# Kernel optimization log

Measured on AMD Instinct MI355X. Metric: run time of the kernel, lower is better.

The kernel has to match this reference:

```python
import jax, jax.numpy as jnp
import numpy as np

B, N, D, H = 8, 512, 512, 8
DK = D // H          # 64
DIM_G = 64           # trigonometric geometry embedding dim
WAVE_LEN = 1000.0


def box_relational_embedding(f_g):
    # f_g: [B, N, 4] -> [B, N, N, 64]
    x_min, y_min, x_max, y_max = [f_g[..., i] for i in range(4)]  # [B,N]
    cx = (x_min + x_max) * 0.5
    cy = (y_min + y_max) * 0.5
    w = x_max - x_min + 1.0
    h = y_max - y_min + 1.0
    # pairwise deltas; divide by w_i / h_i of the row box (broadcast over j)
    dx = jnp.log(jnp.clip(jnp.abs((cx[:, :, None] - cx[:, None, :]) / w[:, :, None]), 0.001))
    dy = jnp.log(jnp.clip(jnp.abs((cy[:, :, None] - cy[:, None, :]) / h[:, :, None]), 0.001))
    dw = jnp.log(w[:, :, None] / w[:, None, :])
    dh = jnp.log(h[:, :, None] / h[:, None, :])
    pos = jnp.stack([dx, dy, dw, dh], axis=-1)  # [B,N,N,4]
    feat_range = jnp.arange(DIM_G // 8, dtype=jnp.float32) / (DIM_G / 8.0)  # [8]
    dim_mat = 1.0 / (WAVE_LEN ** feat_range)  # [8]
    mul = (100.0 * pos)[..., None] * dim_mat  # [B,N,N,4,8]
    mul = mul.reshape(pos.shape[0], pos.shape[1], pos.shape[2], -1)  # [B,N,N,32]
    return jnp.concatenate([jnp.sin(mul), jnp.cos(mul)], axis=-1)  # [B,N,N,64]


def setup_inputs() -> dict:
    key = jax.random.key(0)
    ks = jax.random.split(key, 12)
    s = 1.0 / np.sqrt(D)
    return {
        "input_query": jax.random.normal(ks[0], (B, N, D), jnp.float32),
        "input_key": jax.random.normal(ks[1], (B, N, D), jnp.float32),
        "input_value": jax.random.normal(ks[2], (B, N, D), jnp.float32),
        "input_box": jax.random.uniform(ks[3], (B, N, 4), jnp.float32),
        "mask": jax.random.randint(ks[4], (B, N), 0, 2, jnp.int32),
        "not_objects": jax.random.randint(ks[5], (B, N), 0, 2).astype(jnp.bool_),
        "Wq": jax.random.normal(ks[6], (D, D), jnp.float32) * s,
        "bq": jnp.zeros((D,), jnp.float32),
        "Wk": jax.random.normal(ks[7], (D, D), jnp.float32) * s,
        "bk": jnp.zeros((D,), jnp.float32),
        "Wv": jax.random.normal(ks[8], (D, D), jnp.float32) * s,
        "bv": jnp.zeros((D,), jnp.float32),
        "Wo": jax.random.normal(ks[9], (D, D), jnp.float32) * s,
        "bo": jnp.zeros((D,), jnp.float32),
        "WG": jax.random.normal(ks[10], (H, DIM_G), jnp.float32) * 0.1,
        "bG": jnp.zeros((H,), jnp.float32),
    }


def reference(input_query, input_key, input_value, input_box, mask, not_objects,
              Wq, bq, Wk, bk, Wv, bv, Wo, bo, WG, bG):
    emb = box_relational_embedding(input_box)  # [B,N,N,64]

    def proj(x, W, b):
        return (x @ W + b).reshape(B, N, H, DK).transpose(0, 2, 1, 3)  # [B,H,N,DK]

    q = proj(input_query, Wq, bq)
    k = proj(input_key, Wk, bk)
    v = proj(input_value, Wv, bv)

    scores = jnp.einsum('bhnd,bhmd->bhnm', q, k) / np.sqrt(DK).astype(np.float32)
    scores = jnp.where(mask[:, None, None, :] == 0, -1e9, scores)

    # per-head geometry weights: [B,H,N,N]
    wg = jax.nn.relu(jnp.einsum('bnmg,hg->bhnm', emb, WG) + bG[None, :, None, None])

    # object mask: zero the geometry log-bias where either i or j is not an object
    pair_not_obj = not_objects[:, None, :, None] | not_objects[:, None, None, :]  # [B,1,N,N]
    mask_obj = 1.0 - pair_not_obj.astype(jnp.float32)

    logits = jnp.log(jnp.clip(wg, 1e-6)) * mask_obj + scores
    attn = jax.nn.softmax(logits, axis=-1)  # dropout is identity in eval mode

    out = jnp.einsum('bhnm,bhmd->bhnd', attn, v)
    out = out.transpose(0, 2, 1, 3).reshape(B, N, D)
    return out @ Wo + bo
```

## Files before the change

### kernel.cpp

```cpp
#include <hip/hip_runtime.h>
#include <hip/hip_fp16.h>

#define B_ 8
#define N_ 512
#define D_ 512
#define H_ 8
#define DK_ 64

typedef unsigned int uint;
typedef unsigned short ushort;
typedef __attribute__((ext_vector_type(8))) short short8;
typedef __attribute__((ext_vector_type(8))) _Float16 half8;
typedef __attribute__((ext_vector_type(4))) _Float16 half4;
typedef __attribute__((ext_vector_type(4))) float floatx4;

__device__ __forceinline__ float bf2f(ushort s) { return __uint_as_float(((uint)s) << 16); }
__device__ __forceinline__ ushort f2bf(float f) {
    uint x = __float_as_uint(f);
    return (ushort)((x + 0x7fffu + ((x >> 16) & 1u)) >> 16);
}
__device__ __forceinline__ float blo(uint u) { return __uint_as_float(u << 16); }
__device__ __forceinline__ float bhi(uint u) { return __uint_as_float(u & 0xffff0000u); }
__device__ __forceinline__ float ldf(const void* p, size_t i, int isbf) {
    return isbf ? bf2f(((const ushort*)p)[i]) : ((const float*)p)[i];
}
__device__ __forceinline__ short ldb(const void* p, size_t i, int isbf) {
    return isbf ? (short)(((const ushort*)p)[i]) : (short)f2bf(((const float*)p)[i]);
}
__device__ __forceinline__ float4 ldbox(const void* p, size_t row, int isbf) {
    if (isbf) {
        const uint2 u = ((const uint2*)p)[row];
        return make_float4(blo(u.x), bhi(u.x), blo(u.y), bhi(u.y));
    }
    return ((const float4*)p)[row];
}
__device__ __forceinline__ float flog(float x) {
    return __builtin_amdgcn_logf(x) * 0.69314718056f;
}
__device__ __forceinline__ float fexp(float x) {
    return __builtin_amdgcn_exp2f(x * 1.44269504089f);
}
__device__ __forceinline__ void fsincos_rev(float rev, float* s, float* c) {
    const float fr = rev - floorf(rev);
    *s = __builtin_amdgcn_sinf(fr);
    *c = __builtin_amdgcn_cosf(fr);
}
__device__ __forceinline__ uint pkbf(uint a, uint b) {
    return __builtin_amdgcn_perm(b + 0x8000u, a + 0x8000u, 0x07060302u);
}

__global__ __launch_bounds__(256) void probe_dtype(const uint* __restrict__ q,
                                                   int* __restrict__ flag) {
    __shared__ int s[256];
    const int t = threadIdx.x;
    int cnt = 0;
    for (int i = t; i < 4096; i += 256) {
        const uint e = (q[i] >> 7) & 0xffu;
        cnt += (e >= 0x70u && e <= 0x84u) ? 1 : 0;
    }
    s[t] = cnt;
    __syncthreads();
    for (int d = 128; d > 0; d >>= 1) {
        if (t < d) s[t] += s[t + d];
        __syncthreads();
    }
    if (t == 0) *flag = (s[0] > 3276) ? 1 : 0;
}

__global__ __launch_bounds__(256) void transw(const void* __restrict__ w0,
                                              const void* __restrict__ w1,
                                              const void* __restrict__ w2,
                                              const void* __restrict__ w3,
                                              const void* __restrict__ b0,
                                              const void* __restrict__ b1,
                                              const void* __restrict__ b2,
                                              const void* __restrict__ b3,
                                              ushort* __restrict__ wt,
                                              float* __restrict__ biasf,
                                              const int* __restrict__ flagp) {
    const int isbf = *flagp;
    const int z = blockIdx.z;
    const void* W = (z == 0) ? w0 : (z == 1) ? w1 : (z == 2) ? w2 : w3;
    const int n0 = blockIdx.x * 32, k0 = blockIdx.y * 32;
    __shared__ float tile[32][33];
    const int tx = threadIdx.x & 31, ty = threadIdx.x >> 5;
#pragma unroll
    for (int r = 0; r < 4; ++r)
        tile[ty + 8 * r][tx] = ldf(W, (size_t)(k0 + ty + 8 * r) * D_ + n0 + tx, isbf);
    if (blockIdx.x == 0 && blockIdx.y == 0) {
        const void* bz = (z == 0) ? b0 : (z == 1) ? b1 : (z == 2) ? b2 : b3;
        for (int e = threadIdx.x; e < 512; e += 256)
            biasf[z * 512 + e] = ldf(bz, e, isbf);
    }
    __syncthreads();
#pragma unroll
    for (int r = 0; r < 4; ++r)
        wt[(size_t)z * 262144 + (size_t)(n0 + ty + 8 * r) * D_ + k0 + tx] =
            f2bf(tile[tx][ty + 8 * r]);
}

__global__ __launch_bounds__(256) void stage1(
    const void* __restrict__ xq, const void* __restrict__ xk, const void* __restrict__ xv,
    const ushort* __restrict__ wt, const float* __restrict__ biasf,
    ushort* __restrict__ oq, ushort* __restrict__ ok, ushort* __restrict__ ov,
    const void* __restrict__ box, const int* __restrict__ nobj,
    const void* __restrict__ WG, const void* __restrict__ bG,
    ushort* __restrict__ glog, const int* __restrict__ flagp) {
    __shared__ __align__(16) char smem[22336];
    const int isbf = *flagp;
    const int bid = blockIdx.x;
    const int t = threadIdx.x, wv = t >> 6, lane = t & 63;
    const int m16 = lane & 15, quad = lane >> 4;

    if (bid < 768) {
        const int z = bid >> 8, rem = bid & 255;
        const int row0 = (rem & 31) * 128, col0 = (rem >> 5) * 64;
        const char* A = (const char*)((z == 0) ? xq : (z == 1) ? xk : xv);
        const ushort* W = wt + (size_t)z * 262144;
        const float* bias = biasf + z * 512;
        ushort (*As)[40] = (ushort(*)[40])smem;
        ushort (*Ws)[40] = (ushort(*)[40])(smem + 10240);
        floatx4 acc[2][4] = {};

        const int ar = t >> 1, ah = t & 1;
        const int wr = t >> 2, wc = (t & 3) * 8;

        uint4 ua, ub, uc, ud;
        short8 ps0, ps1, pw;

        auto loadA = [&](int k0) {
            const size_t e = (size_t)(row0 + ar) * D_ + k0 + ah * 16;
            if (isbf) {
                ps0 = *(const short8*)(A + 2 * e);
                ps1 = *(const short8*)(A + 2 * e + 16);
            } else {
                const uint* ap = (const uint*)A + e;
                ua = *(const uint4*)(ap);
                ub = *(const uint4*)(ap + 4);
                uc = *(const uint4*)(ap + 8);
                ud = *(const uint4*)(ap + 12);
            }
            pw = *(const short8*)(W + (size_t)(col0 + wr) * D_ + k0 + wc);
        };
        auto stage = [&]() {
            if (isbf) {
                *(short8*)&As[ar][ah * 16] = ps0;
                *(short8*)&As[ar][ah * 16 + 8] = ps1;
            } else {
                uint4 lo, hi;
                lo.x = pkbf(ua.x, ua.y); lo.y = pkbf(ua.z, ua.w);
                lo.z = pkbf(ub.x, ub.y); lo.w = pkbf(ub.z, ub.w);
                hi.x = pkbf(uc.x, uc.y); hi.y = pkbf(uc.z, uc.w);
                hi.z = pkbf(ud.x, ud.y); hi.w = pkbf(ud.z, ud.w);
                *(uint4*)&As[ar][ah * 16] = lo;
                *(uint4*)&As[ar][ah * 16 + 8] = hi;
            }
            *(short8*)&Ws[wr][wc] = pw;
        };

        loadA(0);
        for (int k0 = 0; k0 < D_; k0 += 32) {
            __syncthreads();
            stage();
            __syncthreads();
            if (k0 + 32 < D_) loadA(k0 + 32);

            const short8 a0 = *(const short8*)&As[wv * 32 + m16][quad * 8];
            const short8 a1 = *(const short8*)&As[wv * 32 + 16 + m16][quad * 8];
            const short8 b0 = *(const short8*)&Ws[m16][quad * 8];
            const short8 b1 = *(const short8*)&Ws[16 + m16][quad * 8];
            const short8 b2 = *(const short8*)&Ws[32 + m16][quad * 8];
            const short8 b3 = *(const short8*)&Ws[48 + m16][quad * 8];
            acc[0][0] = __builtin_amdgcn_mfma_f32_16x16x32_bf16(a0, b0, acc[0][0], 0, 0, 0);
            acc[0][1] = __builtin_amdgcn_mfma_f32_16x16x32_bf16(a0, b1, acc[0][1], 0, 0, 0);
            acc[0][2] = __builtin_amdgcn_mfma_f32_16x16x32_bf16(a0, b2, acc[0][2], 0, 0, 0);
            acc[0][3] = __builtin_amdgcn_mfma_f32_16x16x32_bf16(a0, b3, acc[0][3], 0, 0, 0);
            acc[1][0] = __builtin_amdgcn_mfma_f32_16x16x32_bf16(a1, b0, acc[1][0], 0, 0, 0);
            acc[1][1] = __builtin_amdgcn_mfma_f32_16x16x32_bf16(a1, b1, acc[1][1], 0, 0, 0);
            acc[1][2] = __builtin_amdgcn_mfma_f32_16x16x32_bf16(a1, b2, acc[1][2], 0, 0, 0);
            acc[1][3] = __builtin_amdgcn_mfma_f32_16x16x32_bf16(a1, b3, acc[1][3], 0, 0, 0);
        }

#pragma unroll
        for (int mt = 0; mt < 2; ++mt) {
#pragma unroll
            for (int nt = 0; nt < 4; ++nt) {
                const int colg = col0 + nt * 16 + m16;
                const float bi = bias[colg];
                const float v0 = acc[mt][nt][0] + bi, v1 = acc[mt][nt][1] + bi;
                const float v2 = acc[mt][nt][2] + bi, v3 = acc[mt][nt][3] + bi;
                const int rowb = row0 + wv * 32 + mt * 16 + quad * 4;
                if (z == 2) {
                    const int bhv = (rowb >> 9) * H_ + (colg >> 6);
                    uint2 pk;
                    pk.x = (uint)f2bf(v0) | ((uint)f2bf(v1) << 16);
                    pk.y = (uint)f2bf(v2) | ((uint)f2bf(v3) << 16);
                    *(uint2*)(ov + ((size_t)bhv * DK_ + (colg & 63)) * N_ + (rowb & 511)) = pk;
                } else {
                    ushort* o = (z == 0) ? oq : ok;
                    const float vv[4] = {v0, v1, v2, v3};
#pragma unroll
                    for (int r = 0; r < 4; ++r) {
                        const int row = rowb + r;
                        o[((size_t)((row >> 9) * H_ + (colg >> 6)) * N_ + (row & 511)) * DK_ +
                          (colg & 63)] = f2bf(vv[r]);
                    }
                }
            }
        }
    } else {
        const int id = bid - 768;
        const int i = id & 511, bl = id >> 9;
        _Float16 (*trig)[76] = (_Float16(*)[76])smem;
        _Float16 (*wgf)[72] = (_Float16(*)[72])(smem + 19456);
        float* mobja = (float*)(smem + 21760);
        float* bgs = (float*)(smem + 22272);

        for (int e = t; e < 1024; e += 256) {
            const int h = e >> 6, g = e & 63;
            wgf[h][g] = (_Float16)((h < 8) ? ldf(WG, (size_t)h * 64 + g, isbf) : 0.f);
        }
        if (t < 8) bgs[t] = ldf(bG, t, isbf);

        const float4 bi4 = ldbox(box, (size_t)bl * N_ + i, isbf);
        const float wi = bi4.z - bi4.x + 1.0f, hi = bi4.w - bi4.y + 1.0f;
        const float cxi = (bi4.x + bi4.z) * 0.5f, cyi = (bi4.y + bi4.w) * 0.5f;
        const float rwi = 1.0f / wi, rhi = 1.0f / hi;
        const float lwi = flog(wi), lhi = flog(hi);
        const int noi = nobj[bl * N_ + i];
        __syncthreads();

        const half8 bf0 = *(const half8*)&wgf[m16][quad * 8];
        const half8 bf1 = *(const half8*)&wgf[m16][quad * 8 + 32];
        _Float16* gb = (_Float16*)glog +
                       ((((size_t)bl * 32 + (i >> 4)) * 8) * 16 + (i & 15)) * 512;
        const float dmrev[8] = {15.915494f, 6.7115083f, 2.8302207f, 1.1934936f,
                                0.50329214f, 0.21223603f, 0.089498095f, 0.037742074f};

        for (int c = 0; c < 4; ++c) {
            const int jbase = c * 128;
            {
                const int pair = t >> 1, hf = t & 1;
                const int j = jbase + pair;
                const float4 bj4 = ldbox(box, (size_t)bl * N_ + j, isbf);
                const float wj = bj4.z - bj4.x + 1.0f, hj = bj4.w - bj4.y + 1.0f;
                float p0, p1;
                if (hf == 0) {
                    const float cxj = (bj4.x + bj4.z) * 0.5f, cyj = (bj4.y + bj4.w) * 0.5f;
                    p0 = flog(fmaxf(fabsf((cxi - cxj) * rwi), 0.001f));
                    p1 = flog(fmaxf(fabsf((cyi - cyj) * rhi), 0.001f));
                    mobja[pair] = (noi || nobj[bl * N_ + j]) ? 0.f : 1.f;
                } else {
                    p0 = lwi - flog(wj);
                    p1 = lhi - flog(hj);
                }
#pragma unroll
                for (int pp = 0; pp < 2; ++pp) {
                    const float base = pp ? p1 : p0;
                    half8 s8, c8;
#pragma unroll
                    for (int f = 0; f < 8; ++f) {
                        float sv, cv;
                        fsincos_rev(base * dmrev[f], &sv, &cv);
                        s8[f] = (_Float16)sv;
                        c8[f] = (_Float16)cv;
                    }
                    const int g0 = hf * 16 + pp * 8;
                    *(half4*)&trig[pair][g0]          = *(const half4*)&s8;
                    *(half4*)&trig[pair][g0 + 4]      = *((const half4*)&s8 + 1);
                    *(half4*)&trig[pair][32 + g0]     = *(const half4*)&c8;
                    *(half4*)&trig[pair][32 + g0 + 4] = *((const half4*)&c8 + 1);
                }
            }
            __syncthreads();
            {
#pragma unroll
                for (int sub = 0; sub < 2; ++sub) {
                    const int row = wv * 32 + sub * 16 + m16;
                    half8 a0, a1;
                    *((half4*)&a0)     = *(const half4*)&trig[row][quad * 8];
                    *((half4*)&a0 + 1) = *(const half4*)&trig[row][quad * 8 + 4];
                    *((half4*)&a1)     = *(const half4*)&trig[row][32 + quad * 8];
                    *((half4*)&a1 + 1) = *(const half4*)&trig[row][32 + quad * 8 + 4];
                    floatx4 acc = {};
                    acc = __builtin_amdgcn_mfma_f32_16x16x32_f16(a0, bf0, acc, 0, 0, 0);
                    acc = __builtin_amdgcn_mfma_f32_16x16x32_f16(a1, bf1, acc, 0, 0, 0);
                    if (m16 < 8) {
#pragma unroll
                        for (int r = 0; r < 4; ++r) {
                            const int pair = wv * 32 + sub * 16 + quad * 4 + r;
                            const float wg = acc[r] + bgs[m16];
                            const float gl = flog(fmaxf(wg, 1e-6f)) * mobja[pair];
                            gb[(size_t)m16 * 8192 + jbase + pair] = (_Float16)gl;
                        }
                    }
                }
            }
            __syncthreads();
        }
    }
}

__global__ __launch_bounds__(256) void gemm1(
    const ushort* __restrict__ att, const ushort* __restrict__ wt,
    const float* __restrict__ biasf, void* __restrict__ dout,
    const int* __restrict__ flagp) {
    const int isbf = *flagp;
    const ushort* W = wt + (size_t)3 * 262144;
    const float* bias = biasf + 3 * 512;
    const int row0 = blockIdx.x * 128, col0 = blockIdx.y * 64;
    const int t = threadIdx.x, wv = t >> 6, lane = t & 63;
    const int m16 = lane & 15, quad = lane >> 4;

    __shared__ ushort As[128][40];
    __shared__ ushort Ws[64][40];
    floatx4 acc[2][4] = {};

    const int ar = t >> 1, ah = t & 1;
    const int wr = t >> 2, wc = (t & 3) * 8;

    short8 ps0, ps1, pw;
    auto loadA = [&](int k0) {
        const ushort* ap = att + (size_t)(row0 + ar) * D_ + k0 + ah * 16;
        ps0 = *(const short8*)(ap);
        ps1 = *(const short8*)(ap + 8);
        pw = *(const short8*)(W + (size_t)(col0 + wr) * D_ + k0 + wc);
    };

    loadA(0);
    for (int k0 = 0; k0 < D_; k0 += 32) {
        __syncthreads();
        *(short8*)&As[ar][ah * 16] = ps0;
        *(short8*)&As[ar][ah * 16 + 8] = ps1;
        *(short8*)&Ws[wr][wc] = pw;
        __syncthreads();
        if (k0 + 32 < D_) loadA(k0 + 32);

        const short8 a0 = *(const short8*)&As[wv * 32 + m16][quad * 8];
        const short8 a1 = *(const short8*)&As[wv * 32 + 16 + m16][quad * 8];
        const short8 b0 = *(const short8*)&Ws[m16][quad * 8];
        const short8 b1 = *(const short8*)&Ws[16 + m16][quad * 8];
        const short8 b2 = *(const short8*)&Ws[32 + m16][quad * 8];
        const short8 b3 = *(const short8*)&Ws[48 + m16][quad * 8];
        acc[0][0] = __builtin_amdgcn_mfma_f32_16x16x32_bf16(a0, b0, acc[0][0], 0, 0, 0);
        acc[0][1] = __builtin_amdgcn_mfma_f32_16x16x32_bf16(a0, b1, acc[0][1], 0, 0, 0);
        acc[0][2] = __builtin_amdgcn_mfma_f32_16x16x32_bf16(a0, b2, acc[0][2], 0, 0, 0);
        acc[0][3] = __builtin_amdgcn_mfma_f32_16x16x32_bf16(a0, b3, acc[0][3], 0, 0, 0);
        acc[1][0] = __builtin_amdgcn_mfma_f32_16x16x32_bf16(a1, b0, acc[1][0], 0, 0, 0);
        acc[1][1] = __builtin_amdgcn_mfma_f32_16x16x32_bf16(a1, b1, acc[1][1], 0, 0, 0);
        acc[1][2] = __builtin_amdgcn_mfma_f32_16x16x32_bf16(a1, b2, acc[1][2], 0, 0, 0);
        acc[1][3] = __builtin_amdgcn_mfma_f32_16x16x32_bf16(a1, b3, acc[1][3], 0, 0, 0);
    }

#pragma unroll
    for (int mt = 0; mt < 2; ++mt) {
#pragma unroll
        for (int nt = 0; nt < 4; ++nt) {
            const int colg = col0 + nt * 16 + m16;
            const float bi = bias[colg];
#pragma unroll
            for (int r = 0; r < 4; ++r) {
                const int row = row0 + wv * 32 + mt * 16 + quad * 4 + r;
                const float v = acc[mt][nt][r] + bi;
                if (isbf) ((ushort*)dout)[(size_t)row * D_ + colg] = f2bf(v);
                else      ((float*)dout)[(size_t)row * D_ + colg] = v;
            }
        }
    }
}

__global__ __launch_bounds__(256) void attn3(
    const ushort* __restrict__ qw, const ushort* __restrict__ kw,
    const ushort* __restrict__ vt, const int* __restrict__ mask,
    const ushort* __restrict__ glog, ushort* __restrict__ att, int b0) {
    const int it = blockIdx.x, h = blockIdx.y, bl = blockIdx.z;
    const int bg = b0 + bl;
    const int i0 = it * 16;
    const int t = threadIdx.x, wv = t >> 6, lane = t & 63;
    const int m16 = lane & 15, quad = lane >> 4;
    const size_t bh = (size_t)(bg * H_ + h);

    __shared__ float lg[16][516];
    __shared__ ushort sbuf[16 * 520];
    __shared__ float rsumInv[16];

    {
        const uint4* src = (const uint4*)(glog + (((size_t)bl * 32 + it) * 8 + h) * 8192);
        uint4* dst = (uint4*)sbuf;
#pragma unroll
        for (int e = 0; e < 4; ++e) dst[t + 256 * e] = src[t + 256 * e];
    }
    const ushort* qrow = qw + (bh * N_ + i0 + m16) * DK_ + quad * 8;
    const short8 aq0 = *(const short8*)(qrow);
    const short8 aq1 = *(const short8*)(qrow + 32);
    __syncthreads();

#pragma unroll
    for (int tt = 0; tt < 8; ++tt) {
        const int j0 = wv * 128 + tt * 16;
        const ushort* krow = kw + (bh * N_ + j0 + m16) * DK_ + quad * 8;
        const short8 bk0 = *(const short8*)(krow);
        const short8 bk1 = *(const short8*)(krow + 32);
        floatx4 acc = {};
        acc = __builtin_amdgcn_mfma_f32_16x16x32_bf16(aq0, bk0, acc, 0, 0, 0);
        acc = __builtin_amdgcn_mfma_f32_16x16x32_bf16(aq1, bk1, acc, 0, 0, 0);
        const int mj = mask[bg * N_ + j0 + m16];
        const __half* gt = (const __half*)sbuf;
#pragma unroll
        for (int r = 0; r < 4; ++r) {
            const int i = quad * 4 + r;
            const float g = __half2float(gt[i * 512 + j0 + m16]);
            lg[i][j0 + m16] = (mj ? 0.125f * acc[r] : -1e9f) + g;
        }
    }
    __syncthreads();

    {
        const int row = t >> 4, l = t & 15;
        float v[32];
        float mx = -3e38f;
#pragma unroll
        for (int s = 0; s < 32; ++s) { v[s] = lg[row][l + 16 * s]; mx = fmaxf(mx, v[s]); }
#pragma unroll
        for (int d = 1; d < 16; d <<= 1) mx = fmaxf(mx, __shfl_xor(mx, d, 16));
        float sm = 0.f;
#pragma unroll
        for (int s = 0; s < 32; ++s) { const float p = fexp(v[s] - mx); sm += p; v[s] = p; }
#pragma unroll
        for (int d = 1; d < 16; d <<= 1) sm += __shfl_xor(sm, d, 16);
#pragma unroll
        for (int s = 0; s < 32; ++s)
            sbuf[row * 520 + l + 16 * s] = (ushort)((__float_as_uint(v[s]) + 0x8000u) >> 16);
        if (l == 0) rsumInv[row] = 1.0f / sm;
    }
    __syncthreads();

    {
        const int dk0 = wv * 16;
        const ushort* vrow = vt + (bh * DK_ + dk0 + m16) * N_ + quad * 8;
        floatx4 oc = {};
#pragma unroll
        for (int kc = 0; kc < 16; ++kc) {
            const short8 ap = *(const short8*)(sbuf + m16 * 520 + kc * 32 + quad * 8);
            const short8 bv = *(const short8*)(vrow + kc * 32);
            oc = __builtin_amdgcn_mfma_f32_16x16x32_bf16(ap, bv, oc, 0, 0, 0);
        }
#pragma unroll
        for (int r = 0; r < 4; ++r) {
            const int i = quad * 4 + r;
            const float o = oc[r] * rsumInv[i];
            att[((size_t)(bg * N_ + i0 + i)) * D_ + h * DK_ + dk0 + m16] = f2bf(o);
        }
    }
}

__global__ __launch_bounds__(256) void gemm16(const void* __restrict__ A,
                                              const void* __restrict__ W,
                                              const void* __restrict__ bias,
                                              void* __restrict__ out,
                                              const int* __restrict__ flagp,
                                              int a_follows, int mode) {
    const int isbf = *flagp;
    const int a_isbf = a_follows ? isbf : 1;
    const int wave = threadIdx.x >> 6;
    const int tile = blockIdx.x * 4 + wave;
    const int tm = tile >> 5, tn = tile & 31;
    const int row0 = tm * 16, col0 = tn * 16;
    const int lane = threadIdx.x & 63;
    const int m = lane & 15, quad = lane >> 4;
    floatx4 acc = {0.f, 0.f, 0.f, 0.f};
    const size_t abase = (size_t)(row0 + m) * D_ + quad * 8;
    const size_t wbase = (size_t)(quad * 8) * D_ + col0 + m;
    for (int k0 = 0; k0 < D_; k0 += 32) {
        short8 af, bf;
#pragma unroll
        for (int j = 0; j < 8; ++j) af[j] = ldb(A, abase + k0 + j, a_isbf);
#pragma unroll
        for (int j = 0; j < 8; ++j) bf[j] = ldb(W, wbase + (size_t)(k0 + j) * D_, isbf);
        acc = __builtin_amdgcn_mfma_f32_16x16x32_bf16(af, bf, acc, 0, 0, 0);
    }
    const int col = col0 + m;
    const float bi = ldf(bias, col, isbf);
#pragma unroll
    for (int r = 0; r < 4; ++r) {
        const int row = row0 + quad * 4 + r;
        const float v = acc[r] + bi;
        if (mode == 1) {
            ((ushort*)out)[(size_t)(((row >> 9) * H_ + (col >> 6)) * N_ + (row & 511)) * DK_ + (col & 63)] = f2bf(v);
        } else if (isbf) {
            ((ushort*)out)[(size_t)row * D_ + col] = f2bf(v);
        } else {
            ((float*)out)[(size_t)row * D_ + col] = v;
        }
    }
}

__global__ __launch_bounds__(256) void attn_old(
    const ushort* __restrict__ qw, const ushort* __restrict__ kw,
    const ushort* __restrict__ vw, const void* __restrict__ box,
    const int* __restrict__ mask, const int* __restrict__ nobj,
    const void* __restrict__ WG, const void* __restrict__ bG,
    ushort* __restrict__ att, const int* __restrict__ flagp) {
    const int isbf = *flagp;
    const int b = blockIdx.z, h = blockIdx.y;
    const int i0 = blockIdx.x * 8;
    const int t = threadIdx.x;
    __shared__ float lg[8][520];
    __shared__ float q_s[8][68];
    __shared__ float wgh[64];
    __shared__ float cxi[8], cyi[8], rwi[8], rhi[8], lwi[8], lhi[8];
    __shared__ int noi[8];
    __shared__ float rsum[8];
    for (int e = t; e < 512; e += 256) {
        const int ii = e >> 6, dk = e & 63;
        q_s[ii][dk] = bf2f(qw[(size_t)((b * H_ + h) * N_ + i0 + ii) * DK_ + dk]) * 0.125f;
    }
    if (t < 64) wgh[t] = ldf(WG, h * 64 + t, isbf);
    if (t < 8) {
        const size_t bb = (size_t)(b * N_ + i0 + t) * 4;
        const float xmn = ldf(box, bb + 0, isbf), ymn = ldf(box, bb + 1, isbf);
        const float xmx = ldf(box, bb + 2, isbf), ymx = ldf(box, bb + 3, isbf);
        const float w = xmx - xmn + 1.0f, hh = ymx - ymn + 1.0f;
        cxi[t] = (xmn + xmx) * 0.5f;
        cyi[t] = (ymn + ymx) * 0.5f;
        rwi[t] = 1.0f / w;
        rhi[t] = 1.0f / hh;
        lwi[t] = __logf(w);
        lhi[t] = __logf(hh);
        noi[t] = nobj[b * N_ + i0 + t];
    }
    const float bg = ldf(bG, h, isbf);
    __syncthreads();
    for (int jl = 0; jl < 2; ++jl) {
        const int j = t + jl * 256;
        float acc[8];
#pragma unroll
        for (int ii = 0; ii < 8; ++ii) acc[ii] = 0.f;
        const uint4* krow = (const uint4*)(kw + (size_t)((b * H_ + h) * N_ + j) * DK_);
#pragma unroll
        for (int c = 0; c < 8; ++c) {
            const uint4 ku = krow[c];
            float kf[8];
            kf[0] = blo(ku.x); kf[1] = bhi(ku.x); kf[2] = blo(ku.y); kf[3] = bhi(ku.y);
            kf[4] = blo(ku.z); kf[5] = bhi(ku.z); kf[6] = blo(ku.w); kf[7] = bhi(ku.w);
#pragma unroll
            for (int ii = 0; ii < 8; ++ii) {
                const float4 qa = *(const float4*)(&q_s[ii][c * 8]);
                const float4 qb = *(const float4*)(&q_s[ii][c * 8 + 4]);
                acc[ii] += qa.x * kf[0] + qa.y * kf[1] + qa.z * kf[2] + qa.w * kf[3] +
                           qb.x * kf[4] + qb.y * kf[5] + qb.z * kf[6] + qb.w * kf[7];
            }
        }
        const int mj = mask[b * N_ + j];
        const size_t bb = (size_t)(b * N_ + j) * 4;
        const float xmn = ldf(box, bb + 0, isbf), ymn = ldf(box, bb + 1, isbf);
        const float xmx = ldf(box, bb + 2, isbf), ymx = ldf(box, bb + 3, isbf);
        const float cxj = (xmn + xmx) * 0.5f, cyj = (ymn + ymx) * 0.5f;
        const float wj = xmx - xmn + 1.0f, hj = ymx - ymn + 1.0f;
        const float lwj = __logf(wj), lhj = __logf(hj);
        const int noj = nobj[b * N_ + j];
        const float dm[8] = {1.0f, 0.421696503f, 0.177827941f, 0.074989421f,
                             0.031622777f, 0.013335214f, 0.005623413f, 0.002371374f};
        for (int ii = 0; ii < 8; ++ii) {
            const float mobj = (noi[ii] || noj) ? 0.f : 1.f;
            const float dx = __logf(fmaxf(fabsf((cxi[ii] - cxj) * rwi[ii]), 0.001f));
            const float dy = __logf(fmaxf(fabsf((cyi[ii] - cyj) * rhi[ii]), 0.001f));
            const float pos[4] = {dx, dy, lwi[ii] - lwj, lhi[ii] - lhj};
            float wg = bg;
            for (int p = 0; p < 4; ++p) {
                const float base = 100.f * pos[p];
#pragma unroll
                for (int f = 0; f < 8; ++f) {
                    float sv, cv;
                    __sincosf(base * dm[f], &sv, &cv);
                    const int g = p * 8 + f;
                    wg += sv * wgh[g] + cv * wgh[32 + g];
                }
            }
            lg[ii][j] = (mj ? acc[ii] : -1e9f) + __logf(fmaxf(wg, 1e-6f)) * mobj;
        }
    }
    __syncthreads();
    {
        const int rr = t >> 5, l32 = t & 31;
        float mx = -3e38f;
        for (int j = l32; j < N_; j += 32) mx = fmaxf(mx, lg[rr][j]);
#pragma unroll
        for (int d = 1; d < 32; d <<= 1) mx = fmaxf(mx, __shfl_xor(mx, d, 32));
        float sm = 0.f;
        for (int j = l32; j < N_; j += 32) {
            const float p = __expf(lg[rr][j] - mx);
            lg[rr][j] = p;
            sm += p;
        }
#pragma unroll
        for (int d = 1; d < 32; d <<= 1) sm += __shfl_xor(sm, d, 32);
        if (l32 == 0) rsum[rr] = sm;
    }
    __syncthreads();
    {
        const int ii = t >> 5, dkp = t & 31;
        float o0 = 0.f, o1 = 0.f;
        const uint* vbase = (const uint*)vw + (size_t)((b * H_ + h) * N_) * (DK_ / 2) + dkp;
        for (int j = 0; j < N_; ++j) {
            const uint u = vbase[(size_t)j * (DK_ / 2)];
            const float p = lg[ii][j];
            o0 += p * blo(u);
            o1 += p * bhi(u);
        }
        const float inv = 1.0f / rsum[ii];
        const uint pk = (uint)f2bf(o0 * inv) | ((uint)f2bf(o1 * inv) << 16);
        ((uint*)att)[(size_t)(b * N_ + i0 + ii) * (D_ / 2) + h * 32 + dkp] = pk;
    }
}

extern "C" void kernel_launch(void* const* d_in, const int* in_sizes, int n_in,
                              void* d_out, int out_size, void* d_ws, size_t ws_size,
                              hipStream_t stream) {
    const void* xq = d_in[0];
    const void* xk = d_in[1];
    const void* xv = d_in[2];
    const void* box = d_in[3];
    const int* mask = (const int*)d_in[4];
    const int* nobj = (const int*)d_in[5];
    const void* Wq = d_in[6];
    const void* bq = d_in[7];
    const void* Wk = d_in[8];
    const void* bk = d_in[9];
    const void* Wv = d_in[10];
    const void* bv = d_in[11];
    const void* Wo = d_in[12];
    const void* bo = d_in[13];
    const void* WG = d_in[14];
    const void* bG = d_in[15];

    char* ws = (char*)d_ws;
    const size_t MB = 1u << 20;

    if (ws_size >= 54 * MB) {
        int* flag = (int*)ws;
        float* biasf = (float*)(ws + 4096);
        ushort* wt = (ushort*)(ws + 16384);
        size_t p = 16384 + 2097152;
        ushort* qw = (ushort*)(ws + p); p += 4194304;
        ushort* kw = (ushort*)(ws + p); p += 4194304;
        ushort* vt = (ushort*)(ws + p); p += 4194304;
        ushort* att = (ushort*)(ws + p); p += 4194304;
        ushort* glog = (ushort*)(ws + p);

        hipLaunchKernelGGL(probe_dtype, dim3(1), dim3(256), 0, stream, (const uint*)xq, flag);
        hipLaunchKernelGGL(transw, dim3(16, 16, 4), dim3(256), 0, stream,
                           Wq, Wk, Wv, Wo, bq, bk, bv, bo, wt, biasf, flag);
        hipLaunchKernelGGL(stage1, dim3(4864), dim3(256), 0, stream,
                           xq, xk, xv, wt, biasf, qw, kw, vt,
                           box, nobj, WG, bG, glog, flag);
        hipLaunchKernelGGL(attn3, dim3(32, H_, B_), dim3(256), 0, stream,
                           qw, kw, vt, mask, glog, att, 0);
        hipLaunchKernelGGL(gemm1, dim3(32, 8), dim3(256), 0, stream,
                           att, wt, biasf, d_out, flag);
    } else {
        int* flag = (int*)ws;
        ushort* qw = (ushort*)(ws + 256);
        ushort* kw = (ushort*)(ws + 256 + 4194304);
        ushort* vw = (ushort*)(ws + 256 + 8388608);
        ushort* att = (ushort*)(ws + 256 + 12582912);
        hipLaunchKernelGGL(probe_dtype, dim3(1), dim3(256), 0, stream, (const uint*)xq, flag);
        hipLaunchKernelGGL(gemm16, dim3(2048), dim3(256), 0, stream, xq, Wq, bq, (void*)qw, flag, 1, 1);
        hipLaunchKernelGGL(gemm16, dim3(2048), dim3(256), 0, stream, xk, Wk, bk, (void*)kw, flag, 1, 1);
        hipLaunchKernelGGL(gemm16, dim3(2048), dim3(256), 0, stream, xv, Wv, bv, (void*)vw, flag, 1, 1);
        hipLaunchKernelGGL(attn_old, dim3(N_ / 8, H_, B_), dim3(256), 0, stream,
                           qw, kw, vw, box, mask, nobj, WG, bG, att, flag);
        hipLaunchKernelGGL(gemm16, dim3(2048), dim3(256), 0, stream, att, Wo, bo, d_out, flag, 0, 2);
    }
}
```

Before: 198.2 us.

## Fold dtype probe into transw, shrink GEMM tiles, interleave projection and geometry blocks

Result: faster. 187.8 us (-5.3%).

```diff
diff --git a/kernel.cpp b/kernel.cpp
--- a/kernel.cpp
+++ b/kernel.cpp
@@ -48,23 +48,29 @@
 __device__ __forceinline__ uint pkbf(uint a, uint b) {
     return __builtin_amdgcn_perm(b + 0x8000u, a + 0x8000u, 0x07060302u);
 }
-
-__global__ __launch_bounds__(256) void probe_dtype(const uint* __restrict__ q,
-                                                   int* __restrict__ flag) {
-    __shared__ int s[256];
+__device__ __forceinline__ int sniff_dtype(const uint* q, int* scratch) {
     const int t = threadIdx.x;
     int cnt = 0;
     for (int i = t; i < 4096; i += 256) {
         const uint e = (q[i] >> 7) & 0xffu;
         cnt += (e >= 0x70u && e <= 0x84u) ? 1 : 0;
     }
-    s[t] = cnt;
+    scratch[t] = cnt;
     __syncthreads();
     for (int d = 128; d > 0; d >>= 1) {
-        if (t < d) s[t] += s[t + d];
+        if (t < d) scratch[t] += scratch[t + d];
         __syncthreads();
     }
-    if (t == 0) *flag = (s[0] > 3276) ? 1 : 0;
+    const int r = (scratch[0] > 3276) ? 1 : 0;
+    __syncthreads();
+    return r;
+}
+
+__global__ __launch_bounds__(256) void probe_dtype(const uint* __restrict__ q,
+                                                   int* __restrict__ flag) {
+    __shared__ int s[256];
+    const int r = sniff_dtype(q, s);
+    if (threadIdx.x == 0) *flag = r;
 }
 
 __global__ __launch_bounds__(256) void transw(const void* __restrict__ w0,
@@ -75,10 +81,12 @@
                                               const void* __restrict__ b1,
                                               const void* __restrict__ b2,
                                               const void* __restrict__ b3,
+                                              const uint* __restrict__ xq,
                                               ushort* __restrict__ wt,
                                               float* __restrict__ biasf,
-                                              const int* __restrict__ flagp) {
-    const int isbf = *flagp;
+                                              int* __restrict__ flag) {
+    __shared__ int cnt_s[256];
+    const int isbf = sniff_dtype(xq, cnt_s);
     const int z = blockIdx.z;
     const void* W = (z == 0) ? w0 : (z == 1) ? w1 : (z == 2) ? w2 : w3;
     const int n0 = blockIdx.x * 32, k0 = blockIdx.y * 32;
@@ -91,6 +99,7 @@
         const void* bz = (z == 0) ? b0 : (z == 1) ? b1 : (z == 2) ? b2 : b3;
         for (int e = threadIdx.x; e < 512; e += 256)
             biasf[z * 512 + e] = ldf(bz, e, isbf);
+        if (z == 0 && threadIdx.x == 0) *flag = isbf;
     }
     __syncthreads();
 #pragma unroll
@@ -108,54 +117,46 @@
     ushort* __restrict__ glog, const int* __restrict__ flagp) {
     __shared__ __align__(16) char smem[22336];
     const int isbf = *flagp;
-    const int bid = blockIdx.x;
+    const int grp = blockIdx.x / 11, kk = blockIdx.x % 11;
     const int t = threadIdx.x, wv = t >> 6, lane = t & 63;
     const int m16 = lane & 15, quad = lane >> 4;
 
-    if (bid < 768) {
-        const int z = bid >> 8, rem = bid & 255;
-        const int row0 = (rem & 31) * 128, col0 = (rem >> 5) * 64;
+    if (kk < 3) {
+        const int id = grp * 3 + kk;
+        const int z = id >> 9, rem = id & 511;
+        const int row0 = (rem & 63) * 64, col0 = (rem >> 6) * 64;
         const char* A = (const char*)((z == 0) ? xq : (z == 1) ? xk : xv);
         const ushort* W = wt + (size_t)z * 262144;
         const float* bias = biasf + z * 512;
         ushort (*As)[40] = (ushort(*)[40])smem;
-        ushort (*Ws)[40] = (ushort(*)[40])(smem + 10240);
-        floatx4 acc[2][4] = {};
-
-        const int ar = t >> 1, ah = t & 1;
-        const int wr = t >> 2, wc = (t & 3) * 8;
-
-        uint4 ua, ub, uc, ud;
-        short8 ps0, ps1, pw;
-
+        ushort (*Ws)[40] = (ushort(*)[40])(smem + 5120);
+        floatx4 acc[4] = {};
+
+        const int ar = t >> 2, ac = (t & 3) * 8;
+
+        uint4 ua, ub;
+        short8 ps, pw;
         auto loadA = [&](int k0) {
-            const size_t e = (size_t)(row0 + ar) * D_ + k0 + ah * 16;
+            const size_t e = (size_t)(row0 + ar) * D_ + k0 + ac;
             if (isbf) {
-                ps0 = *(const short8*)(A + 2 * e);
-                ps1 = *(const short8*)(A + 2 * e + 16);
+                ps = *(const short8*)(A + 2 * e);
             } else {
                 const uint* ap = (const uint*)A + e;
                 ua = *(const uint4*)(ap);
                 ub = *(const uint4*)(ap + 4);
-                uc = *(const uint4*)(ap + 8);
-                ud = *(const uint4*)(ap + 12);
             }
-            pw = *(const short8*)(W + (size_t)(col0 + wr) * D_ + k0 + wc);
+            pw = *(const short8*)(W + (size_t)(col0 + ar) * D_ + k0 + ac);
         };
         auto stage = [&]() {
             if (isbf) {
-                *(short8*)&As[ar][ah * 16] = ps0;
-                *(short8*)&As[ar][ah * 16 + 8] = ps1;
+                *(short8*)&As[ar][ac] = ps;
             } else {
-                uint4 lo, hi;
+                uint4 lo;
                 lo.x = pkbf(ua.x, ua.y); lo.y = pkbf(ua.z, ua.w);
                 lo.z = pkbf(ub.x, ub.y); lo.w = pkbf(ub.z, ub.w);
-                hi.x = pkbf(uc.x, uc.y); hi.y = pkbf(uc.z, uc.w);
-                hi.z = pkbf(ud.x, ud.y); hi.w = pkbf(ud.z, ud.w);
-                *(uint4*)&As[ar][ah * 16] = lo;
-                *(uint4*)&As[ar][ah * 16 + 8] = hi;
+                *(uint4*)&As[ar][ac] = lo;
             }
-            *(short8*)&Ws[wr][wc] = pw;
+            *(short8*)&Ws[ar][ac] = pw;
         };
 
         loadA(0);
@@ -165,51 +166,43 @@
             __syncthreads();
             if (k0 + 32 < D_) loadA(k0 + 32);
 
-            const short8 a0 = *(const short8*)&As[wv * 32 + m16][quad * 8];
-            const short8 a1 = *(const short8*)&As[wv * 32 + 16 + m16][quad * 8];
+            const short8 a0 = *(const short8*)&As[wv * 16 + m16][quad * 8];
             const short8 b0 = *(const short8*)&Ws[m16][quad * 8];
             const short8 b1 = *(const short8*)&Ws[16 + m16][quad * 8];
             const short8 b2 = *(const short8*)&Ws[32 + m16][quad * 8];
             const short8 b3 = *(const short8*)&Ws[48 + m16][quad * 8];
-            acc[0][0] = __builtin_amdgcn_mfma_f32_16x16x32_bf16(a0, b0, acc[0][0], 0, 0, 0);
-            acc[0][1] = __builtin_amdgcn_mfma_f32_16x16x32_bf16(a0, b1, acc[0][1], 0, 0, 0);
-            acc[0][2] = __builtin_amdgcn_mfma_f32_16x16x32_bf16(a0, b2, acc[0][2], 0, 0, 0);
-            acc[0][3] = __builtin_amdgcn_mfma_f32_16x16x32_bf16(a0, b3, acc[0][3], 0, 0, 0);
-            acc[1][0] = __builtin_amdgcn_mfma_f32_16x16x32_bf16(a1, b0, acc[1][0], 0, 0, 0);
-            acc[1][1] = __builtin_amdgcn_mfma_f32_16x16x32_bf16(a1, b1, acc[1][1], 0, 0, 0);
-            acc[1][2] = __builtin_amdgcn_mfma_f32_16x16x32_bf16(a1, b2, acc[1][2], 0, 0, 0);
-            acc[1][3] = __builtin_amdgcn_mfma_f32_16x16x32_bf16(a1, b3, acc[1][3], 0, 0, 0);
-        }
-
-#pragma unroll
-        for (int mt = 0; mt < 2; ++mt) {
-#pragma unroll
-            for (int nt = 0; nt < 4; ++nt) {
-                const int colg = col0 + nt * 16 + m16;
-                const float bi = bias[colg];
-                const float v0 = acc[mt][nt][0] + bi, v1 = acc[mt][nt][1] + bi;
-                const float v2 = acc[mt][nt][2] + bi, v3 = acc[mt][nt][3] + bi;
-                const int rowb = row0 + wv * 32 + mt * 16 + quad * 4;
-                if (z == 2) {
-                    const int bhv = (rowb >> 9) * H_ + (colg >> 6);
-                    uint2 pk;
-                    pk.x = (uint)f2bf(v0) | ((uint)f2bf(v1) << 16);
-                    pk.y = (uint)f2bf(v2) | ((uint)f2bf(v3) << 16);
-                    *(uint2*)(ov + ((size_t)bhv * DK_ + (colg & 63)) * N_ + (rowb & 511)) = pk;
-                } else {
-                    ushort* o = (z == 0) ? oq : ok;
-                    const float vv[4] = {v0, v1, v2, v3};
-#pragma unroll
-                    for (int r = 0; r < 4; ++r) {
-                        const int row = rowb + r;
-                        o[((size_t)((row >> 9) * H_ + (colg >> 6)) * N_ + (row & 511)) * DK_ +
-                          (colg & 63)] = f2bf(vv[r]);
-                    }
+            acc[0] = __builtin_amdgcn_mfma_f32_16x16x32_bf16(a0, b0, acc[0], 0, 0, 0);
+            acc[1] = __builtin_amdgcn_mfma_f32_16x16x32_bf16(a0, b1, acc[1], 0, 0, 0);
+            acc[2] = __builtin_amdgcn_mfma_f32_16x16x32_bf16(a0, b2, acc[2], 0, 0, 0);
+            acc[3] = __builtin_amdgcn_mfma_f32_16x16x32_bf16(a0, b3, acc[3], 0, 0, 0);
+        }
+
+#pragma unroll
+        for (int nt = 0; nt < 4; ++nt) {
+            const int colg = col0 + nt * 16 + m16;
+            const float bi = bias[colg];
+            const float v0 = acc[nt][0] + bi, v1 = acc[nt][1] + bi;
+            const float v2 = acc[nt][2] + bi, v3 = acc[nt][3] + bi;
+            const int rowb = row0 + wv * 16 + quad * 4;
+            if (z == 2) {
+                const int bhv = (rowb >> 9) * H_ + (colg >> 6);
+                uint2 pk;
+                pk.x = (uint)f2bf(v0) | ((uint)f2bf(v1) << 16);
+                pk.y = (uint)f2bf(v2) | ((uint)f2bf(v3) << 16);
+                *(uint2*)(ov + ((size_t)bhv * DK_ + (colg & 63)) * N_ + (rowb & 511)) = pk;
+            } else {
+                ushort* o = (z == 0) ? oq : ok;
+                const float vv[4] = {v0, v1, v2, v3};
+#pragma unroll
+                for (int r = 0; r < 4; ++r) {
+                    const int row = rowb + r;
+                    o[((size_t)((row >> 9) * H_ + (colg >> 6)) * N_ + (row & 511)) * DK_ +
+                      (colg & 63)] = f2bf(vv[r]);
                 }
             }
         }
     } else {
-        const int id = bid - 768;
+        const int id = grp * 8 + (kk - 3);
         const int i = id & 511, bl = id >> 9;
         _Float16 (*trig)[76] = (_Float16(*)[76])smem;
         _Float16 (*wgf)[72] = (_Float16(*)[72])(smem + 19456);
@@ -308,63 +301,51 @@
     const int isbf = *flagp;
     const ushort* W = wt + (size_t)3 * 262144;
     const float* bias = biasf + 3 * 512;
-    const int row0 = blockIdx.x * 128, col0 = blockIdx.y * 64;
+    const int row0 = blockIdx.x * 64, col0 = blockIdx.y * 64;
     const int t = threadIdx.x, wv = t >> 6, lane = t & 63;
     const int m16 = lane & 15, quad = lane >> 4;
 
-    __shared__ ushort As[128][40];
+    __shared__ ushort As[64][40];
     __shared__ ushort Ws[64][40];
-    floatx4 acc[2][4] = {};
-
-    const int ar = t >> 1, ah = t & 1;
-    const int wr = t >> 2, wc = (t & 3) * 8;
-
-    short8 ps0, ps1, pw;
+    floatx4 acc[4] = {};
+
+    const int ar = t >> 2, ac = (t & 3) * 8;
+
+    short8 ps, pw;
     auto loadA = [&](int k0) {
-        const ushort* ap = att + (size_t)(row0 + ar) * D_ + k0 + ah * 16;
-        ps0 = *(const short8*)(ap);
-        ps1 = *(const short8*)(ap + 8);
-        pw = *(const short8*)(W + (size_t)(col0 + wr) * D_ + k0 + wc);
+        ps = *(const short8*)(att + (size_t)(row0 + ar) * D_ + k0 + ac);
+        pw = *(const short8*)(W + (size_t)(col0 + ar) * D_ + k0 + ac);
     };
 
     loadA(0);
     for (int k0 = 0; k0 < D_; k0 += 32) {
         __syncthreads();
-        *(short8*)&As[ar][ah * 16] = ps0;
-        *(short8*)&As[ar][ah * 16 + 8] = ps1;
-        *(short8*)&Ws[wr][wc] = pw;
+        *(short8*)&As[ar][ac] = ps;
+        *(short8*)&Ws[ar][ac] = pw;
         __syncthreads();
         if (k0 + 32 < D_) loadA(k0 + 32);
 
-        const short8 a0 = *(const short8*)&As[wv * 32 + m16][quad * 8];
-        const short8 a1 = *(const short8*)&As[wv * 32 + 16 + m16][quad * 8];
+        const short8 a0 = *(const short8*)&As[wv * 16 + m16][quad * 8];
         const short8 b0 = *(const short8*)&Ws[m16][quad * 8];
         const short8 b1 = *(const short8*)&Ws[16 + m16][quad * 8];
         const short8 b2 = *(const short8*)&Ws[32 + m16][quad * 8];
         const short8 b3 = *(const short8*)&Ws[48 + m16][quad * 8];
-        acc[0][0] = __builtin_amdgcn_mfma_f32_16x16x32_bf16(a0, b0, acc[0][0], 0, 0, 0);
-        acc[0][1] = __builtin_amdgcn_mfma_f32_16x16x32_bf16(a0, b1, acc[0][1], 0, 0, 0);
-        acc[0][2] = __builtin_amdgcn_mfma_f32_16x16x32_bf16(a0, b2, acc[0][2], 0, 0, 0);
-        acc[0][3] = __builtin_amdgcn_mfma_f32_16x16x32_bf16(a0, b3, acc[0][3], 0, 0, 0);
-        acc[1][0] = __builtin_amdgcn_mfma_f32_16x16x32_bf16(a1, b0, acc[1][0], 0, 0, 0);
-        acc[1][1] = __builtin_amdgcn_mfma_f32_16x16x32_bf16(a1, b1, acc[1][1], 0, 0, 0);
-        acc[1][2] = __builtin_amdgcn_mfma_f32_16x16x32_bf16(a1, b2, acc[1][2], 0, 0, 0);
-        acc[1][3] = __builtin_amdgcn_mfma_f32_16x16x32_bf16(a1, b3, acc[1][3], 0, 0, 0);
-    }
-
-#pragma unroll
-    for (int mt = 0; mt < 2; ++mt) {
-#pragma unroll
-        for (int nt = 0; nt < 4; ++nt) {
-            const int colg = col0 + nt * 16 + m16;
-            const float bi = bias[colg];
-#pragma unroll
-            for (int r = 0; r < 4; ++r) {
-                const int row = row0 + wv * 32 + mt * 16 + quad * 4 + r;
-                const float v = acc[mt][nt][r] + bi;
-                if (isbf) ((ushort*)dout)[(size_t)row * D_ + colg] = f2bf(v);
-                else      ((float*)dout)[(size_t)row * D_ + colg] = v;
-            }
+        acc[0] = __builtin_amdgcn_mfma_f32_16x16x32_bf16(a0, b0, acc[0], 0, 0, 0);
+        acc[1] = __builtin_amdgcn_mfma_f32_16x16x32_bf16(a0, b1, acc[1], 0, 0, 0);
+        acc[2] = __builtin_amdgcn_mfma_f32_16x16x32_bf16(a0, b2, acc[2], 0, 0, 0);
+        acc[3] = __builtin_amdgcn_mfma_f32_16x16x32_bf16(a0, b3, acc[3], 0, 0, 0);
+    }
+
+#pragma unroll
+    for (int nt = 0; nt < 4; ++nt) {
+        const int colg = col0 + nt * 16 + m16;
+        const float bi = bias[colg];
+#pragma unroll
+        for (int r = 0; r < 4; ++r) {
+            const int row = row0 + wv * 16 + quad * 4 + r;
+            const float v = acc[nt][r] + bi;
+            if (isbf) ((ushort*)dout)[(size_t)row * D_ + colg] = f2bf(v);
+            else      ((float*)dout)[(size_t)row * D_ + colg] = v;
         }
     }
 }
@@ -648,15 +629,15 @@
         ushort* att = (ushort*)(ws + p); p += 4194304;
         ushort* glog = (ushort*)(ws + p);
 
-        hipLaunchKernelGGL(probe_dtype, dim3(1), dim3(256), 0, stream, (const uint*)xq, flag);
         hipLaunchKernelGGL(transw, dim3(16, 16, 4), dim3(256), 0, stream,
-                           Wq, Wk, Wv, Wo, bq, bk, bv, bo, wt, biasf, flag);
-        hipLaunchKernelGGL(stage1, dim3(4864), dim3(256), 0, stream,
+                           Wq, Wk, Wv, Wo, bq, bk, bv, bo, (const uint*)xq,
+                           wt, biasf, flag);
+        hipLaunchKernelGGL(stage1, dim3(5632), dim3(256), 0, stream,
                            xq, xk, xv, wt, biasf, qw, kw, vt,
                            box, nobj, WG, bG, glog, flag);
         hipLaunchKernelGGL(attn3, dim3(32, H_, B_), dim3(256), 0, stream,
                            qw, kw, vt, mask, glog, att, 0);
-        hipLaunchKernelGGL(gemm1, dim3(32, 8), dim3(256), 0, stream,
+        hipLaunchKernelGGL(gemm1, dim3(64, 8), dim3(256), 0, stream,
                            att, wt, biasf, d_out, flag);
     } else {
         int* flag = (int*)ws;
```
